# Performance work log

Hardware: AMD Instinct MI355X
Metric: run time of the kernel (lower is better)

The kernel has to match this reference:

```python
import jax, jax.numpy as jnp
import numpy as np

B, T_H, N, F_P = 16, 24, 256, 6
H, PRED_LEN, F_W = 64, 12, 4


def _build_static(coords):
    # haversine distance matrix -> gaussian kernel -> threshold (epsilon=0.5)
    lon, lat = coords[:, 0], coords[:, 1]
    dlon = lon[None, :] - lon[:, None]
    dlat = lat[None, :] - lat[:, None]
    a = (np.sin(np.radians(dlat / 2)) ** 2
         + np.cos(np.radians(lat[:, None])) * np.cos(np.radians(lat[None, :]))
         * np.sin(np.radians(dlon / 2)) ** 2)
    dist = 2.0 * 6371.0 * np.arcsin(np.sqrt(np.clip(a, 0.0, None)))
    std = dist.flatten().std()
    adj = np.exp(-np.square(dist / std))
    adj[adj < 0.5] = 0.0
    return adj.astype(np.float32)


def setup_inputs() -> dict:
    key = jax.random.key(0)
    ks = jax.random.split(key, 16)
    rng = np.random.default_rng(0)
    coords_np = np.stack([116.0 + rng.uniform(-1.0, 1.0, N),
                          40.0 + rng.uniform(-1.0, 1.0, N)], axis=1).astype(np.float32)
    s = 0.05
    scale_w = jnp.asarray([1.0, 360.0, 10.0, 1.0], jnp.float32)  # [_, dir(deg), speed, _]
    return {
        "history_pollution": jax.random.normal(ks[0], (B, T_H, N, F_P), jnp.float32),
        "history_weather": jax.random.uniform(ks[1], (B, T_H, F_W), jnp.float32) * scale_w,
        "static_adj": jnp.asarray(_build_static(coords_np)),
        "coords": jnp.asarray(coords_np),
        "w_gc1": jax.random.normal(ks[2], (H, F_P), jnp.float32) * s,
        "b_gc1": jax.random.normal(ks[3], (H,), jnp.float32) * s,
        "w_gc2": jax.random.normal(ks[4], (H, H), jnp.float32) * s,
        "b_gc2": jax.random.normal(ks[5], (H,), jnp.float32) * s,
        "w_ih": jax.random.normal(ks[6], (3 * H, H), jnp.float32) * s,
        "w_hh": jax.random.normal(ks[7], (3 * H, H), jnp.float32) * s,
        "b_ih": jax.random.normal(ks[8], (3 * H,), jnp.float32) * s,
        "b_hh": jax.random.normal(ks[9], (3 * H,), jnp.float32) * s,
        "w_m1": jax.random.normal(ks[10], (32, H), jnp.float32) * s,
        "b_m1": jax.random.normal(ks[11], (32,), jnp.float32) * s,
        "w_m2": jax.random.normal(ks[12], (F_P, 32), jnp.float32) * s,
        "b_m2": jax.random.normal(ks[13], (F_P,), jnp.float32) * s,
    }


def _forward(history_pollution, history_weather, static_adj, coords,
             w_gc1, b_gc1, w_gc2, b_gc2, w_ih, w_hh, b_ih, b_hh,
             w_m1, b_m1, w_m2, b_m2):
    Bs, Th, Ns, Fp = history_pollution.shape
    dt = history_pollution.dtype
    eye = jnp.eye(Ns, dtype=dt)
    # station pair angles: vecs[i,j] = coords[j] - coords[i]
    vecs = coords[None, :, :] - coords[:, None, :]
    ang = jnp.arctan2(vecs[..., 1], vecs[..., 0])  # [N,N]

    def gconv(x, adj, w, b):
        wt = adj + eye[None]                         # [B,N,N]
        d = 1.0 / (jnp.sqrt(wt.sum(-1)) + 1e-6)      # [B,N]
        norm = d[:, :, None] * wt * d[:, None, :]    # D^-1/2 W D^-1/2
        return jnp.einsum('bij,bjf->bif', norm, x) @ w.T + b

    def gcb(x, w_out, w_in):
        h1 = jax.nn.relu(gconv(x, w_out, w_gc1, b_gc1))
        return jax.nn.relu(gconv(h1, w_in, w_gc2, b_gc2))

    def gru(h, x):                                   # h,x: [B*N,H]
        gi = x @ w_ih.T + b_ih
        gh = h @ w_hh.T + b_hh
        i_r, i_z, i_n = jnp.split(gi, 3, axis=-1)
        h_r, h_z, h_n = jnp.split(gh, 3, axis=-1)
        r = jax.nn.sigmoid(i_r + h_r)
        z = jax.nn.sigmoid(i_z + h_z)
        n = jnp.tanh(i_n + r * h_n)
        return (1.0 - z) * n + z * h

    def mlp(x):
        return jax.nn.relu(x @ w_m1.T + b_m1) @ w_m2.T + b_m2

    def enc_step(carry, xs):
        h, _ = carry
        x_t, spd, wd = xs                            # [B,N,F],[B],[B]
        rad = jnp.deg2rad(wd)
        w_dyn = jnp.maximum(spd[:, None, None] * jnp.cos(ang[None] - rad[:, None, None]), 0.0)
        w_out = static_adj[None] * w_dyn             # [B,N,N]
        sf = gcb(x_t, w_out, jnp.swapaxes(w_out, 1, 2))
        h = gru(h, sf.reshape(Bs * Ns, -1))
        return (h, w_out), None

    h0 = jnp.zeros((Bs * Ns, w_hh.shape[1]), dt)
    xs = (jnp.moveaxis(history_pollution, 1, 0),      # [T,B,N,F]
          history_weather[:, :, 2].T,                 # wind speed [T,B]
          history_weather[:, :, 1].T)                 # wind dir   [T,B]
    (h, last_w_out), _ = jax.lax.scan(enc_step, (h0, jnp.zeros((Bs, Ns, Ns), dt)), xs)
    last_w_in = jnp.swapaxes(last_w_out, 1, 2)

    dec0 = mlp(h.reshape(Bs, Ns, -1))

    def dec_step(carry, _):
        h_c, x = carry
        sf = gcb(x, last_w_out, last_w_in)
        h_c = gru(h_c, sf.reshape(Bs * Ns, -1))
        pred = mlp(h_c.reshape(Bs, Ns, -1))
        return (h_c, pred), pred

    _, preds = jax.lax.scan(dec_step, (h, dec0), None, length=PRED_LEN)
    return jnp.moveaxis(preds, 0, 1)                  # [B, pred_len, N, F_P]


def reference(history_pollution, history_weather, static_adj, coords,
              w_gc1, b_gc1, w_gc2, b_gc2, w_ih, w_hh, b_ih, b_hh,
              w_m1, b_m1, w_m2, b_m2):
    return _forward(history_pollution, history_weather, static_adj, coords,
                    w_gc1, b_gc1, w_gc2, b_gc2, w_ih, w_hh, b_ih, b_hh,
                    w_m1, b_m1, w_m2, b_m2)
```

## Files before the change

### kernel.cpp

```cpp
#include <hip/hip_runtime.h>
#include <math.h>

#define Bsz 16
#define Tt 24
#define Nn 256
#define Fp 6
#define Hh 64
#define PredL 12
#define Fw 4
#define M1 32
#define TCHUNK 12
#define DEG2RAD 0.017453292519943295f
#define IDX2(t, b) ((t) * Bsz + (b))

__global__ __launch_bounds__(256) void k_prep(
    const float* __restrict__ coords, const float* __restrict__ adj,
    const float* __restrict__ wgc2, const float* __restrict__ wih,
    const float* __restrict__ whh,  const float* __restrict__ wm1,
    const float* __restrict__ wm2,
    float2* __restrict__ pk,
    float* __restrict__ wgc2T, float* __restrict__ wm1T, float* __restrict__ wm2T,
    float4* __restrict__ wihP, float4* __restrict__ whhP) {
  int tid = threadIdx.x;
  if (blockIdx.x < Nn) {
    int i = blockIdx.x;
    int j = tid;
    float dx = coords[2 * j]     - coords[2 * i];
    float dy = coords[2 * j + 1] - coords[2 * i + 1];
    float ang = atan2f(dy, dx);
    float a = adj[i * Nn + j];
    pk[i * Nn + j] = make_float2(a * cosf(ang), a * sinf(ang));
    return;
  }
  for (int idx = tid; idx < Hh * Hh; idx += 256) {
    int g = idx / Hh, k = idx % Hh;
    wgc2T[k * Hh + g] = wgc2[g * Hh + k];
  }
  for (int idx = tid; idx < M1 * Hh; idx += 256) {
    int m = idx / Hh, k = idx % Hh;
    wm1T[k * M1 + m] = wm1[m * Hh + k];
  }
  for (int idx = tid; idx < Fp * M1; idx += 256) {
    int f = idx / M1, m = idx % M1;
    wm2T[m * Fp + f] = wm2[f * M1 + m];
  }
  for (int idx = tid; idx < Hh * 64; idx += 256) {
    int k = idx >> 6, lane = idx & 63;
    wihP[idx] = make_float4(wih[(0 * 64 + lane) * Hh + k],
                            wih[(1 * 64 + lane) * Hh + k],
                            wih[(2 * 64 + lane) * Hh + k], 0.f);
    whhP[idx] = make_float4(whh[(0 * 64 + lane) * Hh + k],
                            whh[(1 * 64 + lane) * Hh + k],
                            whh[(2 * 64 + lane) * Hh + k], 0.f);
  }
}

__global__ __launch_bounds__(256) void k_enc(
    const float2* __restrict__ pk, const float* __restrict__ hp,
    const float* __restrict__ hw,
    const float* __restrict__ wgc1, const float* __restrict__ bgc1,
    const float* __restrict__ wgc2T, const float* __restrict__ bgc2,
    float* __restrict__ sf_all,
    float* __restrict__ d23, float* __restrict__ e23) {
  __shared__ float d_lds[Nn];
  __shared__ float e_lds[Nn];
  __shared__ __align__(16) float u_s[Nn * 8];
  __shared__ __align__(16) float h1_s[Nn * 68];
  int tb = blockIdx.x, t = tb / Bsz, b = tb % Bsz;
  int tid = threadIdx.x;
  int i = tid;
  float spd = hw[(b * Tt + t) * Fw + 2];
  float rad = hw[(b * Tt + t) * Fw + 1] * DEG2RAD;
  float scr = spd * cosf(rad), ssr = spd * sinf(rad);

  {
    float rs = 0.f, cs = 0.f;
#pragma unroll 4
    for (int j = 0; j < Nn; ++j) {
      float2 pv = pk[j * Nn + i];
      float v = pv.x * scr + pv.y * ssr;
      cs += fmaxf(v, 0.f);
      rs += fmaxf(-v, 0.f);
    }
    float2 pd = pk[i * Nn + i];
    float vii = pd.x * scr + pd.y * ssr;
    rs += vii;
    float di = 1.f / (sqrtf(rs + 1.f) + 1e-6f);
    float ei = 1.f / (sqrtf(cs + 1.f) + 1e-6f);
    d_lds[i] = di; e_lds[i] = ei;
    if (t == Tt - 1) { d23[b * Nn + i] = di; e23[b * Nn + i] = ei; }
  }
  __syncthreads();

  {
    const float* xsrc = hp + (long)(b * Tt + t) * Nn * Fp;
    for (int idx = tid; idx < Nn * Fp; idx += 256) {
      int j = idx / Fp, f = idx - j * Fp;
      u_s[j * 8 + f] = d_lds[j] * xsrc[idx];
    }
    u_s[tid * 8 + 6] = 0.f;
    u_s[tid * 8 + 7] = 0.f;
  }
  __syncthreads();

  {
    float a0 = 0.f, a1 = 0.f, a2 = 0.f, a3 = 0.f, a4 = 0.f, a5 = 0.f;
#pragma unroll 2
    for (int j = 0; j < Nn; ++j) {
      float2 pv = pk[j * Nn + i];
      float v = pv.x * scr + pv.y * ssr;
      float w = fmaxf(-v, 0.f);
      float4 ul = *(const float4*)&u_s[j * 8];
      float4 uh = *(const float4*)&u_s[j * 8 + 4];
      a0 += w * ul.x; a1 += w * ul.y; a2 += w * ul.z;
      a3 += w * ul.w; a4 += w * uh.x; a5 += w * uh.y;
    }
    float2 pd = pk[i * Nn + i];
    float vii = pd.x * scr + pd.y * ssr;
    float di = d_lds[i], ei = e_lds[i];
    float c1 = vii + 1.f;
    float y0 = di * (a0 + c1 * u_s[i * 8 + 0]);
    float y1 = di * (a1 + c1 * u_s[i * 8 + 1]);
    float y2 = di * (a2 + c1 * u_s[i * 8 + 2]);
    float y3 = di * (a3 + c1 * u_s[i * 8 + 3]);
    float y4 = di * (a4 + c1 * u_s[i * 8 + 4]);
    float y5 = di * (a5 + c1 * u_s[i * 8 + 5]);
#pragma unroll
    for (int g4 = 0; g4 < 16; ++g4) {
      float4 hv;
#pragma unroll
      for (int q = 0; q < 4; ++q) {
        int g = g4 * 4 + q;
        float v2 = bgc1[g] + wgc1[g * Fp + 0] * y0 + wgc1[g * Fp + 1] * y1 +
                   wgc1[g * Fp + 2] * y2 + wgc1[g * Fp + 3] * y3 +
                   wgc1[g * Fp + 4] * y4 + wgc1[g * Fp + 5] * y5;
        ((float*)&hv)[q] = fmaxf(v2, 0.f) * ei;
      }
      *(float4*)&h1_s[i * 68 + g4 * 4] = hv;
    }
  }
  __syncthreads();

  float z[64];
#pragma unroll
  for (int k = 0; k < 64; ++k) z[k] = 0.f;
#pragma unroll 2
  for (int j = 0; j < Nn; ++j) {
    float2 pv = pk[j * Nn + i];
    float v = pv.x * scr + pv.y * ssr;
    float wf = fmaxf(v, 0.f) + ((j == i) ? 1.f : 0.f);
#pragma unroll
    for (int g4 = 0; g4 < 16; ++g4) {
      float4 h4 = *(const float4*)&h1_s[j * 68 + g4 * 4];
      z[g4 * 4 + 0] += wf * h4.x;
      z[g4 * 4 + 1] += wf * h4.y;
      z[g4 * 4 + 2] += wf * h4.z;
      z[g4 * 4 + 3] += wf * h4.w;
    }
  }
  {
    float ei = e_lds[i];
#pragma unroll
    for (int k = 0; k < 64; ++k) z[k] *= ei;
  }
  __syncthreads();

#pragma unroll
  for (int c = 0; c < 4; ++c) {
    float s[16];
#pragma unroll
    for (int q = 0; q < 16; ++q) s[q] = bgc2[c * 16 + q];
#pragma unroll
    for (int k = 0; k < 64; ++k) {
      float zk = z[k];
#pragma unroll
      for (int q = 0; q < 16; ++q) s[q] += wgc2T[k * Hh + c * 16 + q] * zk;
    }
#pragma unroll
    for (int q4 = 0; q4 < 4; ++q4) {
      float4 sv = make_float4(fmaxf(s[q4 * 4 + 0], 0.f), fmaxf(s[q4 * 4 + 1], 0.f),
                              fmaxf(s[q4 * 4 + 2], 0.f), fmaxf(s[q4 * 4 + 3], 0.f));
      *(float4*)&h1_s[i * 68 + c * 16 + q4 * 4] = sv;
    }
  }
  __syncthreads();
  long base = (long)IDX2(t, b) * Nn * Hh;
  for (int idx = tid; idx < Nn * 16; idx += 256) {
    int j = idx >> 4, g4 = idx & 15;
    *(float4*)&sf_all[base + j * Hh + g4 * 4] = *(const float4*)&h1_s[j * 68 + g4 * 4];
  }
}

__global__ __launch_bounds__(256) void k_gi(
    const float* __restrict__ sf_all, const float4* __restrict__ wihP,
    const float* __restrict__ bih, float* __restrict__ gi, int t0) {
  __shared__ float sf_c[4][16][64];
  int tid = threadIdx.x, w = tid >> 6, lane = tid & 63;
  int rowc0 = blockIdx.x * 64 + w * 16;
  long rowg0 = (long)t0 * (Bsz * Nn) + rowc0;
#pragma unroll
  for (int rr = 0; rr < 16; ++rr)
    sf_c[w][rr][lane] = sf_all[(rowg0 + rr) * Hh + lane];
  float bi_r = bih[lane], bi_z = bih[64 + lane], bi_n = bih[128 + lane];
  float ar[16], az[16], an[16];
#pragma unroll
  for (int rr = 0; rr < 16; ++rr) { ar[rr] = bi_r; az[rr] = bi_z; an[rr] = bi_n; }
#pragma unroll 2
  for (int kb = 0; kb < 16; ++kb) {
    int k0 = kb * 4;
    float4 wi0 = wihP[(k0 + 0) * 64 + lane];
    float4 wi1 = wihP[(k0 + 1) * 64 + lane];
    float4 wi2 = wihP[(k0 + 2) * 64 + lane];
    float4 wi3 = wihP[(k0 + 3) * 64 + lane];
#pragma unroll
    for (int rr = 0; rr < 16; ++rr) {
      const float4 s4 = *(const float4*)&sf_c[w][rr][k0];
      ar[rr] += s4.x * wi0.x + s4.y * wi1.x + s4.z * wi2.x + s4.w * wi3.x;
      az[rr] += s4.x * wi0.y + s4.y * wi1.y + s4.z * wi2.y + s4.w * wi3.y;
      an[rr] += s4.x * wi0.z + s4.y * wi1.z + s4.z * wi2.z + s4.w * wi3.z;
    }
  }
#pragma unroll
  for (int rr = 0; rr < 16; ++rr) {
    long rowc = rowc0 + rr;
    gi[(rowc * 3 + 0) * 64 + lane] = ar[rr];
    gi[(rowc * 3 + 1) * 64 + lane] = az[rr];
    gi[(rowc * 3 + 2) * 64 + lane] = an[rr];
  }
}

__global__ __launch_bounds__(256) void k_gru_scan4(
    const float* __restrict__ gi, const float4* __restrict__ whhP,
    const float* __restrict__ bhh, float* __restrict__ hstate,
    int t0, int nt) {
  __shared__ float h_s[16][64];
  int b = blockIdx.x >> 4;
  int i0 = (blockIdx.x & 15) * 16;
  int tid = threadIdx.x, w = tid >> 6, lane = tid & 63;
  float bh_r = bhh[lane], bh_z = bhh[64 + lane], bh_n = bhh[128 + lane];
  float h_reg[4];
#pragma unroll
  for (int rr = 0; rr < 4; ++rr) {
    float hv = (t0 == 0) ? 0.f
                         : hstate[((long)b * Nn + i0 + w * 4 + rr) * Hh + lane];
    h_reg[rr] = hv;
    h_s[w * 4 + rr][lane] = hv;
  }
  for (int tl = 0; tl < nt; ++tl) {
    long rbase = ((long)tl * Bsz + b) * Nn + i0 + w * 4;
    float gr[4], gz[4], gn[4], hr[4], hz[4], hn[4];
#pragma unroll
    for (int rr = 0; rr < 4; ++rr) {
      gr[rr] = gi[((rbase + rr) * 3 + 0) * 64 + lane];
      gz[rr] = gi[((rbase + rr) * 3 + 1) * 64 + lane];
      gn[rr] = gi[((rbase + rr) * 3 + 2) * 64 + lane];
      hr[rr] = bh_r; hz[rr] = bh_z; hn[rr] = bh_n;
    }
#pragma unroll 4
    for (int kb = 0; kb < 16; ++kb) {
      int k0 = kb * 4;
      float4 wh0 = whhP[(k0 + 0) * 64 + lane];
      float4 wh1 = whhP[(k0 + 1) * 64 + lane];
      float4 wh2 = whhP[(k0 + 2) * 64 + lane];
      float4 wh3 = whhP[(k0 + 3) * 64 + lane];
#pragma unroll
      for (int rr = 0; rr < 4; ++rr) {
        const float4 h4 = *(const float4*)&h_s[w * 4 + rr][k0];
        hr[rr] += h4.x * wh0.x + h4.y * wh1.x + h4.z * wh2.x + h4.w * wh3.x;
        hz[rr] += h4.x * wh0.y + h4.y * wh1.y + h4.z * wh2.y + h4.w * wh3.y;
        hn[rr] += h4.x * wh0.z + h4.y * wh1.z + h4.z * wh2.z + h4.w * wh3.z;
      }
    }
#pragma unroll
    for (int rr = 0; rr < 4; ++rr) {
      float rg = 1.f / (1.f + expf(-(gr[rr] + hr[rr])));
      float zg = 1.f / (1.f + expf(-(gz[rr] + hz[rr])));
      float ng = tanhf(gn[rr] + rg * hn[rr]);
      float hv = (1.f - zg) * ng + zg * h_reg[rr];
      h_reg[rr] = hv;
      h_s[w * 4 + rr][lane] = hv;
    }
  }
#pragma unroll
  for (int rr = 0; rr < 4; ++rr)
    hstate[((long)b * Nn + i0 + w * 4 + rr) * Hh + lane] = h_reg[rr];
}

__global__ __launch_bounds__(256) void k_misc(
    const float* __restrict__ hw, const float2* __restrict__ pk,
    const float* __restrict__ d23, const float* __restrict__ e23,
    float* __restrict__ A1d, float* __restrict__ A2d,
    const float* __restrict__ hstate,
    const float* __restrict__ wm1T, const float* __restrict__ bm1,
    const float* __restrict__ wm2T, const float* __restrict__ bm2,
    float* __restrict__ xnext) {
  __shared__ float h_lds[16][Hh];
  __shared__ float u_lds[16][M1];
  int tid = threadIdx.x;
  if (blockIdx.x < Bsz * Nn) {
    int b = blockIdx.x >> 8;
    int i = blockIdx.x & 255;
    int j = tid;
    float spd = hw[(b * Tt + (Tt - 1)) * Fw + 2];
    float rad = hw[(b * Tt + (Tt - 1)) * Fw + 1] * DEG2RAD;
    float cr = cosf(rad), sr = sinf(rad);
    const float* drow = d23 + b * Nn;
    const float* erow = e23 + b * Nn;
    float2 pv = pk[i * Nn + j];
    float val = spd * (pv.x * cr + pv.y * sr);
    float dlt = (j == i) ? 1.f : 0.f;
    float wout = fmaxf(val, 0.f);
    float win  = (j == i) ? wout : fmaxf(-val, 0.f);
    A1d[((long)b * Nn + i) * Nn + j] = drow[i] * (wout + dlt) * drow[j];
    A2d[((long)b * Nn + i) * Nn + j] = erow[i] * (win + dlt) * erow[j];
    return;
  }
  int r0 = (blockIdx.x - Bsz * Nn) * 16;
#pragma unroll
  for (int c = 0; c < 4; ++c) {
    int idx = tid + c * 256;
    h_lds[idx >> 6][idx & 63] = hstate[(long)r0 * Hh + idx];
  }
  __syncthreads();
#pragma unroll
  for (int rep = 0; rep < 2; ++rep) {
    int idx = tid + rep * 256;
    int row = idx >> 5, m = idx & 31;
    float um = bm1[m];
    for (int k = 0; k < Hh; ++k) um += wm1T[k * M1 + m] * h_lds[row][k];
    u_lds[row][m] = fmaxf(um, 0.f);
  }
  __syncthreads();
  if (tid < 16 * Fp) {
    int row = tid / Fp, f = tid % Fp;
    float pf = bm2[f];
#pragma unroll
    for (int m = 0; m < M1; ++m) pf += wm2T[m * Fp + f] * u_lds[row][m];
    xnext[(r0 + row) * Fp + f] = pf;
  }
}

__global__ __launch_bounds__(256) void k_dstep_A(
    const float* __restrict__ xb, const float* __restrict__ A1d,
    const float* __restrict__ wgc1, const float* __restrict__ bgc1,
    float* __restrict__ h1d) {
  __shared__ float x_lds[Nn * Fp];
  int b = blockIdx.x >> 5;
  int i0 = (blockIdx.x & 31) * 8;
  int tid = threadIdx.x, w = tid >> 6, lane = tid & 63;
  const float* xsrc = xb + (long)b * Nn * Fp;
#pragma unroll
  for (int c = 0; c < 6; ++c) x_lds[tid + 256 * c] = xsrc[tid + 256 * c];
  __syncthreads();
#pragma unroll
  for (int rr = 0; rr < 2; ++rr) {
    int i = i0 + w * 2 + rr;
    const float* arow = A1d + ((long)b * Nn + i) * Nn;
    float acc[Fp] = {0.f, 0.f, 0.f, 0.f, 0.f, 0.f};
#pragma unroll
    for (int c = 0; c < 4; ++c) {
      int j = lane + 64 * c;
      float wt = arow[j];
#pragma unroll
      for (int f = 0; f < Fp; ++f) acc[f] += wt * x_lds[j * Fp + f];
    }
#pragma unroll
    for (int f = 0; f < Fp; ++f) {
#pragma unroll
      for (int off = 32; off; off >>= 1) acc[f] += __shfl_xor(acc[f], off);
    }
    float hv = bgc1[lane];
#pragma unroll
    for (int f = 0; f < Fp; ++f) hv += wgc1[lane * Fp + f] * acc[f];
    h1d[((long)b * Nn + i) * Hh + lane] = fmaxf(hv, 0.f);
  }
}

__global__ __launch_bounds__(256) void k_dstep_B(
    const float* __restrict__ A2d, const float* __restrict__ h1d,
    const float* __restrict__ wgc2T, const float* __restrict__ bgc2,
    const float4* __restrict__ wihP, const float4* __restrict__ whhP,
    const float* __restrict__ bih, const float* __restrict__ bhh,
    float* __restrict__ hstate,
    const float* __restrict__ wm1T, const float* __restrict__ bm1,
    const float* __restrict__ wm2T, const float* __restrict__ bm2,
    float* __restrict__ outp, float* __restrict__ xnext, int p) {
  __shared__ __align__(16) float wvT[Nn * 12];
  __shared__ float red[4][8][Hh];
  __shared__ float y2[8][Hh];
  __shared__ float sf_s[8][Hh];
  __shared__ float h_s[8][Hh];
  __shared__ float hn_lds[8][Hh];
  __shared__ float u_lds[8][M1];
  int b = blockIdx.x >> 5;
  int i0 = (blockIdx.x & 31) * 8;
  int tid = threadIdx.x, w = tid >> 6, lane = tid & 63;

#pragma unroll
  for (int r = 0; r < 8; ++r)
    wvT[tid * 12 + r] = A2d[((long)b * Nn + i0 + r) * Nn + tid];
  float hp_reg[2];
#pragma unroll
  for (int rr = 0; rr < 2; ++rr) {
    hp_reg[rr] = hstate[((long)b * Nn + i0 + w * 2 + rr) * Hh + lane];
    h_s[w * 2 + rr][lane] = hp_reg[rr];
  }
  __syncthreads();

  float acc[8];
#pragma unroll
  for (int r = 0; r < 8; ++r) acc[r] = 0.f;
  const float* h1b = h1d + (long)b * Nn * Hh;
#pragma unroll 4
  for (int jj = 0; jj < 64; ++jj) {
    int j = w * 64 + jj;
    float hv = h1b[j * Hh + lane];
    float4 w0 = *(const float4*)&wvT[j * 12];
    float4 w1 = *(const float4*)&wvT[j * 12 + 4];
    acc[0] += w0.x * hv; acc[1] += w0.y * hv; acc[2] += w0.z * hv; acc[3] += w0.w * hv;
    acc[4] += w1.x * hv; acc[5] += w1.y * hv; acc[6] += w1.z * hv; acc[7] += w1.w * hv;
  }
#pragma unroll
  for (int r = 0; r < 8; ++r) red[w][r][lane] = acc[r];
  __syncthreads();
#pragma unroll
  for (int rr = 0; rr < 2; ++rr) {
    int r = w * 2 + rr;
    y2[r][lane] = red[0][r][lane] + red[1][r][lane] + red[2][r][lane] + red[3][r][lane];
  }
  {
    float a0 = bgc2[lane], a1 = a0;
    for (int k = 0; k < Hh; ++k) {
      float wk = wgc2T[k * Hh + lane];
      a0 += wk * y2[w * 2 + 0][k];
      a1 += wk * y2[w * 2 + 1][k];
    }
    sf_s[w * 2 + 0][lane] = fmaxf(a0, 0.f);
    sf_s[w * 2 + 1][lane] = fmaxf(a1, 0.f);
  }

  float hn_reg[2];
  {
    float bi_r = bih[lane], bi_z = bih[64 + lane], bi_n = bih[128 + lane];
    float bh_r = bhh[lane], bh_z = bhh[64 + lane], bh_n = bhh[128 + lane];
    float gir[2], giz[2], gin[2], ghr[2], ghz[2], ghn[2];
#pragma unroll
    for (int rr = 0; rr < 2; ++rr) {
      gir[rr] = bi_r; giz[rr] = bi_z; gin[rr] = bi_n;
      ghr[rr] = bh_r; ghz[rr] = bh_z; ghn[rr] = bh_n;
    }
#pragma unroll 4
    for (int kb = 0; kb < 16; ++kb) {
      int k0 = kb * 4;
      float4 wi[4], wh[4];
#pragma unroll
      for (int q = 0; q < 4; ++q) {
        wi[q] = wihP[(k0 + q) * 64 + lane];
        wh[q] = whhP[(k0 + q) * 64 + lane];
      }
#pragma unroll
      for (int rr = 0; rr < 2; ++rr) {
        const float4 s4 = *(const float4*)&sf_s[w * 2 + rr][k0];
        const float4 h4 = *(const float4*)&h_s[w * 2 + rr][k0];
        gir[rr] += s4.x * wi[0].x + s4.y * wi[1].x + s4.z * wi[2].x + s4.w * wi[3].x;
        giz[rr] += s4.x * wi[0].y + s4.y * wi[1].y + s4.z * wi[2].y + s4.w * wi[3].y;
        gin[rr] += s4.x * wi[0].z + s4.y * wi[1].z + s4.z * wi[2].z + s4.w * wi[3].z;
        ghr[rr] += h4.x * wh[0].x + h4.y * wh[1].x + h4.z * wh[2].x + h4.w * wh[3].x;
        ghz[rr] += h4.x * wh[0].y + h4.y * wh[1].y + h4.z * wh[2].y + h4.w * wh[3].y;
        ghn[rr] += h4.x * wh[0].z + h4.y * wh[1].z + h4.z * wh[2].z + h4.w * wh[3].z;
      }
    }
#pragma unroll
    for (int rr = 0; rr < 2; ++rr) {
      float rg = 1.f / (1.f + expf(-(gir[rr] + ghr[rr])));
      float zg = 1.f / (1.f + expf(-(giz[rr] + ghz[rr])));
      float ng = tanhf(gin[rr] + rg * ghn[rr]);
      hn_reg[rr] = (1.f - zg) * ng + zg * hp_reg[rr];
      hstate[((long)b * Nn + i0 + w * 2 + rr) * Hh + lane] = hn_reg[rr];
      hn_lds[w * 2 + rr][lane] = hn_reg[rr];
    }
  }
  __syncthreads();
  {
    int row = tid >> 5, m = tid & 31;
    float um = bm1[m];
    for (int k = 0; k < Hh; ++k) um += wm1T[k * M1 + m] * hn_lds[row][k];
    u_lds[row][m] = fmaxf(um, 0.f);
  }
  __syncthreads();
  if (tid < 8 * Fp) {
    int row = tid / Fp, f = tid - row * Fp;
    float pf = bm2[f];
#pragma unroll
    for (int m = 0; m < M1; ++m) pf += wm2T[m * Fp + f] * u_lds[row][m];
    int i = i0 + row;
    outp[(((long)b * PredL + p) * Nn + i) * Fp + f] = pf;
    xnext[((long)b * Nn + i) * Fp + f] = pf;
  }
}

extern "C" void kernel_launch(void* const* d_in, const int* in_sizes, int n_in,
                              void* d_out, int out_size, void* d_ws, size_t ws_size,
                              hipStream_t stream) {
  const float* hp     = (const float*)d_in[0];
  const float* hw     = (const float*)d_in[1];
  const float* adj    = (const float*)d_in[2];
  const float* coords = (const float*)d_in[3];
  const float* wgc1   = (const float*)d_in[4];
  const float* bgc1   = (const float*)d_in[5];
  const float* wgc2   = (const float*)d_in[6];
  const float* bgc2   = (const float*)d_in[7];
  const float* wih    = (const float*)d_in[8];
  const float* whh    = (const float*)d_in[9];
  const float* bih    = (const float*)d_in[10];
  const float* bhh    = (const float*)d_in[11];
  const float* wm1    = (const float*)d_in[12];
  const float* bm1    = (const float*)d_in[13];
  const float* wm2    = (const float*)d_in[14];
  const float* bm2    = (const float*)d_in[15];
  float* out = (float*)d_out;

  float* w = (float*)d_ws;
  float2* pk    = (float2*)w; w += Nn * Nn * 2;
  float* d23    = w; w += Bsz * Nn;
  float* e23    = w; w += Bsz * Nn;
  float* hstate = w; w += Bsz * Nn * Hh;
  float* sf_all = w; w += (long)Tt * Bsz * Nn * Hh;
  float* gi_ch  = w; w += (long)TCHUNK * Bsz * Nn * 3 * 64;
  float* h1d    = w; w += Bsz * Nn * Hh;
  float* xb0    = w; w += Bsz * Nn * Fp;
  float* xb1    = w; w += Bsz * Nn * Fp;
  float* A1d    = w; w += Bsz * Nn * Nn;
  float* A2d    = w; w += Bsz * Nn * Nn;
  float* wgc2T  = w; w += Hh * Hh;
  float* wm1T   = w; w += Hh * M1;
  float* wm2T   = w; w += M1 * Fp;
  float4* wihP  = (float4*)w; w += Hh * 64 * 4;
  float4* whhP  = (float4*)w; w += Hh * 64 * 4;

  k_prep<<<Nn + 1, 256, 0, stream>>>(coords, adj, wgc2, wih, whh, wm1, wm2,
                                     pk, wgc2T, wm1T, wm2T, wihP, whhP);
  k_enc<<<Tt * Bsz, 256, 0, stream>>>(pk, hp, hw, wgc1, bgc1, wgc2T, bgc2,
                                      sf_all, d23, e23);
  for (int s = 0; s < Tt / TCHUNK; ++s) {
    int t0 = s * TCHUNK;
    k_gi<<<(TCHUNK * Bsz * Nn) / 64, 256, 0, stream>>>(sf_all, wihP, bih,
                                                       gi_ch, t0);
    k_gru_scan4<<<Bsz * 16, 256, 0, stream>>>(gi_ch, whhP, bhh, hstate,
                                              t0, TCHUNK);
  }
  k_misc<<<Bsz * Nn + Bsz * Nn / 16, 256, 0, stream>>>(
      hw, pk, d23, e23, A1d, A2d, hstate, wm1T, bm1, wm2T, bm2, xb0);

  for (int p = 0; p < PredL; ++p) {
    float* xin  = (p & 1) ? xb1 : xb0;
    float* xout = (p & 1) ? xb0 : xb1;
    k_dstep_A<<<Bsz * 32, 256, 0, stream>>>(xin, A1d, wgc1, bgc1, h1d);
    k_dstep_B<<<Bsz * 32, 256, 0, stream>>>(
        A2d, h1d, wgc2T, bgc2, wihP, whhP, bih, bhh, hstate,
        wm1T, bm1, wm2T, bm2, out, xout, p);
  }
}
```

Before: 659.9 us.

## Register-tile graph aggregation as 4 rows by 16 features per thread

The neighbor aggregation loop now has each thread compute a 4-row by 16-feature tile instead of one full row of 64 features. This cuts the LDS reads of h1_s per FMA, and the four wave-uniform h loads per j become broadcasts, while each thread reads four consecutive pk entries as float4. The result is written back to LDS with a rotated column index to avoid bank conflicts, then re-read per row for the second GCN matmul. This adds an extra LDS round trip and a barrier, and the rotated indexing has to be consistent between the write and the read.

New measurement: 662.4 us. About the same (+0.4%).

```diff
diff --git a/kernel.cpp b/kernel.cpp
--- a/kernel.cpp
+++ b/kernel.cpp
@@ -141,46 +141,78 @@
   }
   __syncthreads();
 
-  float z[64];
-#pragma unroll
-  for (int k = 0; k < 64; ++k) z[k] = 0.f;
+  int w = tid >> 6, rb = tid & 63;
+  int g0 = 16 * w, r0 = 4 * rb;
+  float z[4][16];
+#pragma unroll
+  for (int r = 0; r < 4; ++r)
+#pragma unroll
+    for (int q = 0; q < 16; ++q) z[r][q] = 0.f;
 #pragma unroll 2
   for (int j = 0; j < Nn; ++j) {
-    float2 pv = pk[j * Nn + i];
-    float v = pv.x * scr + pv.y * ssr;
-    float wf = fmaxf(v, 0.f) + ((j == i) ? 1.f : 0.f);
-#pragma unroll
-    for (int g4 = 0; g4 < 16; ++g4) {
-      float4 h4 = *(const float4*)&h1_s[j * 68 + g4 * 4];
-      z[g4 * 4 + 0] += wf * h4.x;
-      z[g4 * 4 + 1] += wf * h4.y;
-      z[g4 * 4 + 2] += wf * h4.z;
-      z[g4 * 4 + 3] += wf * h4.w;
-    }
-  }
-  {
-    float ei = e_lds[i];
-#pragma unroll
-    for (int k = 0; k < 64; ++k) z[k] *= ei;
-  }
-  __syncthreads();
-
-#pragma unroll
-  for (int c = 0; c < 4; ++c) {
-    float s[16];
-#pragma unroll
-    for (int q = 0; q < 16; ++q) s[q] = bgc2[c * 16 + q];
-#pragma unroll
-    for (int k = 0; k < 64; ++k) {
-      float zk = z[k];
-#pragma unroll
-      for (int q = 0; q < 16; ++q) s[q] += wgc2T[k * Hh + c * 16 + q] * zk;
-    }
-#pragma unroll
-    for (int q4 = 0; q4 < 4; ++q4) {
-      float4 sv = make_float4(fmaxf(s[q4 * 4 + 0], 0.f), fmaxf(s[q4 * 4 + 1], 0.f),
-                              fmaxf(s[q4 * 4 + 2], 0.f), fmaxf(s[q4 * 4 + 3], 0.f));
-      *(float4*)&h1_s[i * 68 + c * 16 + q4 * 4] = sv;
+    float4 hA = *(const float4*)&h1_s[j * 68 + g0];
+    float4 hB = *(const float4*)&h1_s[j * 68 + g0 + 4];
+    float4 hC = *(const float4*)&h1_s[j * 68 + g0 + 8];
+    float4 hD = *(const float4*)&h1_s[j * 68 + g0 + 12];
+    const float4* pp = (const float4*)(pk + (long)j * Nn + r0);
+    float4 p01 = pp[0], p23 = pp[1];
+    float wf[4];
+    wf[0] = fmaxf(p01.x * scr + p01.y * ssr, 0.f) + ((j == r0 + 0) ? 1.f : 0.f);
+    wf[1] = fmaxf(p01.z * scr + p01.w * ssr, 0.f) + ((j == r0 + 1) ? 1.f : 0.f);
+    wf[2] = fmaxf(p23.x * scr + p23.y * ssr, 0.f) + ((j == r0 + 2) ? 1.f : 0.f);
+    wf[3] = fmaxf(p23.z * scr + p23.w * ssr, 0.f) + ((j == r0 + 3) ? 1.f : 0.f);
+#pragma unroll
+    for (int r = 0; r < 4; ++r) {
+      float wr = wf[r];
+      z[r][0]  += wr * hA.x; z[r][1]  += wr * hA.y;
+      z[r][2]  += wr * hA.z; z[r][3]  += wr * hA.w;
+      z[r][4]  += wr * hB.x; z[r][5]  += wr * hB.y;
+      z[r][6]  += wr * hB.z; z[r][7]  += wr * hB.w;
+      z[r][8]  += wr * hC.x; z[r][9]  += wr * hC.y;
+      z[r][10] += wr * hC.z; z[r][11] += wr * hC.w;
+      z[r][12] += wr * hD.x; z[r][13] += wr * hD.y;
+      z[r][14] += wr * hD.z; z[r][15] += wr * hD.w;
+    }
+  }
+#pragma unroll
+  for (int r = 0; r < 4; ++r) {
+    float er = e_lds[r0 + r];
+#pragma unroll
+    for (int q = 0; q < 16; ++q) z[r][q] *= er;
+  }
+  __syncthreads();
+
+#pragma unroll
+  for (int r = 0; r < 4; ++r) {
+#pragma unroll
+    for (int q = 0; q < 16; ++q) {
+      h1_s[(r0 + r) * 68 + ((g0 + q + rb) & 63)] = z[r][q];
+    }
+  }
+  __syncthreads();
+
+  {
+    float zr[64];
+#pragma unroll 8
+    for (int c = 0; c < 64; ++c)
+      zr[c] = h1_s[i * 68 + ((c + (i >> 2)) & 63)];
+#pragma unroll
+    for (int c4 = 0; c4 < 4; ++c4) {
+      float s[16];
+#pragma unroll
+      for (int q = 0; q < 16; ++q) s[q] = bgc2[c4 * 16 + q];
+#pragma unroll
+      for (int k = 0; k < 64; ++k) {
+        float zk = zr[k];
+#pragma unroll
+        for (int q = 0; q < 16; ++q) s[q] += wgc2T[k * Hh + c4 * 16 + q] * zk;
+      }
+#pragma unroll
+      for (int q4 = 0; q4 < 4; ++q4) {
+        float4 sv = make_float4(fmaxf(s[q4 * 4 + 0], 0.f), fmaxf(s[q4 * 4 + 1], 0.f),
+                                fmaxf(s[q4 * 4 + 2], 0.f), fmaxf(s[q4 * 4 + 3], 0.f));
+        *(float4*)&h1_s[i * 68 + c4 * 16 + q4 * 4] = sv;
+      }
     }
   }
   __syncthreads();
```
